# Kernel optimization log

Hardware: AMD Instinct MI355X
Metric: run time of the kernel (lower is better)

Reference implementation:

```python
import jax, jax.numpy as jnp
import numpy as np

NQ = 10          # num_qubits
NL = 4           # num_layers (StronglyEntanglingLayers)
DIM = 2 ** NQ    # state-vector dimension = input_linear out features
B = 4096
SEQ = 512
PRED = 96

# ---- static basis-state bookkeeping (wire 0 = most significant bit, as in PennyLane) ----

def _cnot_perm(control, target):
    s = np.arange(DIM)
    bit = (s >> (NQ - 1 - control)) & 1
    return s ^ (bit << (NQ - 1 - target))

def _layer_perms():
    # StronglyEntanglingLayers default ranges: r_l = (l % (n_wires - 1)) + 1,
    # then CNOT(i, (i+r) % n) for i = 0..n-1, applied sequentially.
    perms = []
    for l in range(NL):
        r = (l % (NQ - 1)) + 1
        comp = np.arange(DIM)
        for c in range(NQ):
            g = _cnot_perm(c, (c + r) % NQ)
            comp = comp[g]          # compose: state_new[t] = state_old[comp[t]]
        perms.append(jnp.asarray(comp))
    return perms

PERMS = _layer_perms()

_bits = (np.arange(DIM)[:, None] >> (NQ - 1 - np.arange(NQ))[None, :]) & 1
SIGNS = jnp.asarray(1.0 - 2.0 * _bits, dtype=np.float32)   # [DIM, NQ] PauliZ eigenvalues


def _rot_gates(w):
    # PennyLane Rot(phi, theta, omega) = RZ(omega) @ RY(theta) @ RZ(phi); w: [L, n, 3]
    phi, theta, omega = w[..., 0], w[..., 1], w[..., 2]
    c = jnp.cos(theta / 2)
    s = jnp.sin(theta / 2)
    ep = jnp.exp(0.5j * (phi + omega))   # e^{+i(phi+omega)/2}
    em = jnp.exp(0.5j * (phi - omega))   # e^{+i(phi-omega)/2}
    m00 = jnp.conj(ep) * c
    m01 = -em * s
    m10 = jnp.conj(em) * s
    m11 = ep * c
    return jnp.stack([jnp.stack([m00, m01], -1),
                      jnp.stack([m10, m11], -1)], -2)       # [L, n, 2, 2] complex64


def _apply_1q(psi, U, wire):
    # psi: [B, DIM] complex; apply 2x2 U on `wire`
    b = psi.shape[0]
    left = 2 ** wire
    right = 2 ** (NQ - 1 - wire)
    psi = psi.reshape(b, left, 2, right)
    psi = jnp.einsum('ba,kpaq->kpbq', U, psi)
    return psi.reshape(b, DIM)


def _circuit(psi, q_weights):
    mats = _rot_gates(q_weights)
    for l in range(NL):
        for w in range(NQ):
            psi = _apply_1q(psi, mats[l, w], w)
        psi = psi[:, PERMS[l]]          # composed CNOT ring of this layer
    return psi


def reference(x, W_in, b_in, q_weights, W_out, b_out):
    h = x @ W_in.T + b_in + 1e-6                          # input_linear, then +1e-6
    norm = jnp.linalg.norm(h, axis=-1, keepdims=True)
    psi = (h / norm).astype(jnp.complex64)                # AmplitudeEmbedding(normalize=True)
    psi = _circuit(psi, q_weights)                        # StronglyEntanglingLayers
    probs = psi.real ** 2 + psi.imag ** 2
    expvals = probs @ SIGNS                               # [B, NQ] PauliZ expvals
    return expvals @ W_out.T + b_out                      # output_linear


def setup_inputs() -> dict:
    key = jax.random.key(0)
    ks = jax.random.split(key, 6)
    x = jax.random.normal(ks[0], (B, SEQ), dtype=jnp.float32)
    W_in = jax.random.normal(ks[1], (DIM, SEQ), dtype=jnp.float32) / np.sqrt(SEQ)
    b_in = jax.random.normal(ks[2], (DIM,), dtype=jnp.float32) * 0.01
    q_weights = jax.random.uniform(ks[3], (NL, NQ, 3), dtype=jnp.float32,
                                   minval=0.0, maxval=2.0 * np.pi)
    W_out = jax.random.normal(ks[4], (PRED, NQ), dtype=jnp.float32) / np.sqrt(NQ)
    b_out = jax.random.normal(ks[5], (PRED,), dtype=jnp.float32) * 0.01
    return {"x": x, "W_in": W_in, "b_in": b_in, "q_weights": q_weights,
            "W_out": W_out, "b_out": b_out}
```

## Files before the change

kernel.cpp:

```cpp
#include <hip/hip_runtime.h>
#include <math.h>

#define DIM 1024
#define NQ 10
#define NL 4
#define SEQ 512
#define NROWS 4096
#define PRED 96

typedef unsigned short ushort_t;
typedef unsigned int uint_t;
using half8   = __attribute__((ext_vector_type(8))) _Float16;
using float4v = __attribute__((ext_vector_type(4))) float;

__device__ inline ushort_t f2h(float f) { _Float16 h = (_Float16)f; return *(ushort_t*)&h; }
__device__ inline uint_t pkh(float a, float b) {
    _Float16 ha = (_Float16)a, hb = (_Float16)b;
    return (uint_t)(*(ushort_t*)&ha) | ((uint_t)(*(ushort_t*)&hb) << 16);
}

__device__ inline int permf(int s, int r) {
#pragma unroll
    for (int c = 9; c >= 0; --c) {
        int t = (c + r) % 10;
        s ^= ((s >> (9 - c)) & 1) << (9 - t);
    }
    return s;
}

__global__ __launch_bounds__(64)
void circuit_wave64_kernel(const float* __restrict__ Wi, const float* __restrict__ b_in,
                           const float* __restrict__ qw,
                           ushort_t* __restrict__ Csm_r, ushort_t* __restrict__ Csm_i,
                           float* __restrict__ dr, float* __restrict__ di)
{
    __shared__ float gm[NL * NQ][8];
    __shared__ float2 wscr[1024];

    const int lane = threadIdx.x;
    const int jcol = blockIdx.x;

    if (lane < NL * NQ) {
        float phi = qw[lane * 3 + 0], theta = qw[lane * 3 + 1], omega = qw[lane * 3 + 2];
        float ch = cosf(theta * 0.5f), sh = sinf(theta * 0.5f);
        float a = 0.5f * (phi + omega), b = 0.5f * (phi - omega);
        float ca = cosf(a), sa = sinf(a);
        float cb = cosf(b), sb = sinf(b);
        gm[lane][0] =  ch * ca;  gm[lane][1] = -ch * sa;
        gm[lane][2] = -sh * cb;  gm[lane][3] = -sh * sb;
        gm[lane][4] =  sh * cb;  gm[lane][5] = -sh * sb;
        gm[lane][6] =  ch * ca;  gm[lane][7] =  ch * sa;
    }
    __syncthreads();

    float2 P[16];
    if (jcol < SEQ) {
#pragma unroll
        for (int r = 0; r < 16; ++r)
            P[r] = make_float2(Wi[(size_t)(lane * 16 + r) * SEQ + jcol], 0.f);
    } else {
#pragma unroll
        for (int r = 0; r < 16; ++r)
            P[r] = make_float2(b_in[lane * 16 + r] + 1e-6f, 0.f);
    }

#pragma unroll
    for (int l = 0; l < NL; ++l) {
#pragma unroll
        for (int w = 0; w < NQ; ++w) {
            const float* m = gm[l * NQ + w];
            float m00r = m[0], m00i = m[1], m01r = m[2], m01i = m[3];
            float m10r = m[4], m10i = m[5], m11r = m[6], m11i = m[7];
            if (w <= 5) {
                const int lb = 5 - w;
                const int mask = 1 << lb;
                const int myb = (lane >> lb) & 1;
                float cAr = myb ? m11r : m00r, cAi = myb ? m11i : m00i;
                float cQr = myb ? m10r : m01r, cQi = myb ? m10i : m01i;
#pragma unroll
                for (int r = 0; r < 16; ++r) {
                    float ar = P[r].x, ai = P[r].y;
                    float qr_ = __shfl_xor(ar, mask, 64);
                    float qi_ = __shfl_xor(ai, mask, 64);
                    P[r].x = cAr * ar - cAi * ai + cQr * qr_ - cQi * qi_;
                    P[r].y = cAr * ai + cAi * ar + cQr * qi_ + cQi * qr_;
                }
            } else {
                const int mk = 1 << (9 - w);
#pragma unroll
                for (int r0 = 0; r0 < 16; ++r0) {
                    if (r0 & mk) continue;
                    float2 a0 = P[r0], a1 = P[r0 | mk];
                    float2 n0, n1;
                    n0.x = m00r * a0.x - m00i * a0.y + m01r * a1.x - m01i * a1.y;
                    n0.y = m00r * a0.y + m00i * a0.x + m01r * a1.y + m01i * a1.x;
                    n1.x = m10r * a0.x - m10i * a0.y + m11r * a1.x - m11i * a1.y;
                    n1.y = m10r * a0.y + m10i * a0.x + m11r * a1.y + m11i * a1.x;
                    P[r0] = n0; P[r0 | mk] = n1;
                }
            }
        }
        const int rr = l % (NQ - 1) + 1;
        __syncthreads();
#pragma unroll
        for (int r = 0; r < 16; ++r) wscr[lane * 16 + r] = P[r];
        __syncthreads();
        int pl = permf(lane << 4, rr);
#pragma unroll
        for (int r = 0; r < 16; ++r) {
            int src = pl ^ permf(r, rr);
            P[r] = wscr[src];
        }
    }

    if (jcol < SEQ) {
#pragma unroll
        for (int r = 0; r < 16; ++r) {
            int s = lane * 16 + r;
            Csm_r[(size_t)s * SEQ + jcol] = f2h(P[r].x);
            Csm_i[(size_t)s * SEQ + jcol] = f2h(P[r].y);
        }
    } else {
#pragma unroll
        for (int r = 0; r < 16; ++r) {
            dr[lane * 16 + r] = P[r].x;
            di[lane * 16 + r] = P[r].y;
        }
    }
}

#define GBM 128
#define GBNC 64
#define GBK 32
#define LDA 40
#define LDP 65

__global__ __launch_bounds__(256)
void gemm_fused_kernel(const float* __restrict__ x,
                       const ushort_t* __restrict__ Crt_r, const ushort_t* __restrict__ Crt_i,
                       const float* __restrict__ dr, const float* __restrict__ di,
                       float* __restrict__ part)
{
    __shared__ __align__(16) char lds[GBM * LDP * 4];
    ushort_t* Ash = (ushort_t*)lds;
    ushort_t* Bsr = Ash + GBM * LDA;
    ushort_t* Bsi = Bsr + GBNC * LDA;
    float*    Ps  = (float*)lds;
    __shared__ float drs[GBNC], dis[GBNC];

    const int tid = threadIdx.x;
    const int bm = blockIdx.x, bn = blockIdx.y;
    const int lane = tid & 63, wv = tid >> 6;
    const int n0 = bn * GBNC;

    if (tid < GBNC) { drs[tid] = dr[n0 + tid]; dis[tid] = di[n0 + tid]; }

    float4v accr[2][4], acci[2][4];
#pragma unroll
    for (int a = 0; a < 2; ++a)
#pragma unroll
        for (int b = 0; b < 4; ++b) { accr[a][b] = (float4v)0.f; acci[a][b] = (float4v)0.f; }

    const int sr = tid >> 1, ko = (tid & 1) * 16;
    const float* xa = x + (size_t)(bm * GBM + sr) * SEQ + ko;
    const int bsel = tid >> 7;
    const int nr = (tid & 127) >> 1;
    const int bko = (tid & 1) * 16;
    const ushort_t* bsrc = (bsel ? Crt_i : Crt_r) + (size_t)(n0 + nr) * SEQ + bko;
    ushort_t* bdst = (bsel ? Bsi : Bsr) + nr * LDA + bko;

    const int fm = lane & 15, kq = (lane >> 4) * 8;
    const int wrow = wv * 32;

    for (int k0 = 0; k0 < SEQ; k0 += GBK) {
        float fv[16];
        *(float4*)&fv[0]  = *(const float4*)(xa + k0);
        *(float4*)&fv[4]  = *(const float4*)(xa + k0 + 4);
        *(float4*)&fv[8]  = *(const float4*)(xa + k0 + 8);
        *(float4*)&fv[12] = *(const float4*)(xa + k0 + 12);
        uint_t pk[8];
#pragma unroll
        for (int i = 0; i < 8; ++i) pk[i] = pkh(fv[2 * i], fv[2 * i + 1]);
        *(uint4*)(Ash + sr * LDA + ko)     = make_uint4(pk[0], pk[1], pk[2], pk[3]);
        *(uint4*)(Ash + sr * LDA + ko + 8) = make_uint4(pk[4], pk[5], pk[6], pk[7]);
        uint4 b0 = *(const uint4*)(bsrc + k0);
        uint4 b1 = *(const uint4*)(bsrc + k0 + 8);
        *(uint4*)bdst       = b0;
        *(uint4*)(bdst + 8) = b1;
        __syncthreads();

        half8 ah0 = *(half8*)(Ash + (wrow + fm) * LDA + kq);
        half8 ah1 = *(half8*)(Ash + (wrow + 16 + fm) * LDA + kq);
#pragma unroll
        for (int nt = 0; nt < 4; ++nt) {
            half8 br = *(half8*)(Bsr + (nt * 16 + fm) * LDA + kq);
            half8 bi = *(half8*)(Bsi + (nt * 16 + fm) * LDA + kq);
            accr[0][nt] = __builtin_amdgcn_mfma_f32_16x16x32_f16(ah0, br, accr[0][nt], 0, 0, 0);
            accr[1][nt] = __builtin_amdgcn_mfma_f32_16x16x32_f16(ah1, br, accr[1][nt], 0, 0, 0);
            acci[0][nt] = __builtin_amdgcn_mfma_f32_16x16x32_f16(ah0, bi, acci[0][nt], 0, 0, 0);
            acci[1][nt] = __builtin_amdgcn_mfma_f32_16x16x32_f16(ah1, bi, acci[1][nt], 0, 0, 0);
        }
        __syncthreads();
    }

    const int rq = (lane >> 4) * 4;
#pragma unroll
    for (int mt = 0; mt < 2; ++mt)
#pragma unroll
        for (int nt = 0; nt < 4; ++nt) {
            float drv = drs[nt * 16 + fm], div = dis[nt * 16 + fm];
#pragma unroll
            for (int reg = 0; reg < 4; ++reg) {
                int lrow = wrow + mt * 16 + rq + reg;
                float zr = accr[mt][nt][reg] + drv;
                float zi = acci[mt][nt][reg] + div;
                Ps[lrow * LDP + nt * 16 + fm] = zr * zr + zi * zi;
            }
        }
    __syncthreads();

    {
        const int row = tid >> 1, hh = tid & 1;
        const float* pr = Ps + row * LDP + hh * 32;
        float nrm = 0.f, e0 = 0.f, e1 = 0.f, e2 = 0.f, e3 = 0.f, e4 = 0.f, e5 = 0.f;
#pragma unroll
        for (int i = 0; i < 32; ++i) {
            float p = pr[i];
            int c = hh * 32 + i;
            nrm += p;
            e0 += ((c >> 5) & 1) ? -p : p;
            e1 += ((c >> 4) & 1) ? -p : p;
            e2 += ((c >> 3) & 1) ? -p : p;
            e3 += ((c >> 2) & 1) ? -p : p;
            e4 += ((c >> 1) & 1) ? -p : p;
            e5 += (c & 1) ? -p : p;
        }
        size_t base = ((size_t)(bm * GBM + row) * 32 + (bn * 2 + hh)) * 8;
        part[base + 0] = nrm;
        part[base + 1] = e0; part[base + 2] = e1; part[base + 3] = e2;
        part[base + 4] = e3; part[base + 5] = e4; part[base + 6] = e5;
    }
}

__global__ __launch_bounds__(128)
void finalize_kernel(const float* __restrict__ part, const float* __restrict__ W_out,
                     const float* __restrict__ b_out, float* __restrict__ out)
{
    __shared__ float evf[16];
    const int row = blockIdx.x, tid = threadIdx.x;

    if (tid < 64) {
        float v[11];
        if (tid < 32) {
            const float* p = part + ((size_t)row * 32 + tid) * 8;
            float4 a = *(const float4*)p;
            float4 b = *(const float4*)(p + 4);
            float nrm = a.x;
            int bnn = tid >> 1;
            v[0] = nrm;
            v[1] = (bnn & 8) ? -nrm : nrm;
            v[2] = (bnn & 4) ? -nrm : nrm;
            v[3] = (bnn & 2) ? -nrm : nrm;
            v[4] = (bnn & 1) ? -nrm : nrm;
            v[5] = a.y; v[6] = a.z; v[7] = a.w;
            v[8] = b.x; v[9] = b.y; v[10] = b.z;
        } else {
#pragma unroll
            for (int k = 0; k < 11; ++k) v[k] = 0.f;
        }
#pragma unroll
        for (int m = 16; m; m >>= 1)
#pragma unroll
            for (int k = 0; k < 11; ++k) v[k] += __shfl_xor(v[k], m, 64);
        if (tid == 0) {
            float inv = 1.0f / v[0];
#pragma unroll
            for (int k = 0; k < 10; ++k) evf[k] = v[k + 1] * inv;
        }
    }
    __syncthreads();
    if (tid < PRED) {
        float o = b_out[tid];
#pragma unroll
        for (int k = 0; k < NQ; ++k) o = fmaf(W_out[tid * NQ + k], evf[k], o);
        out[(size_t)row * PRED + tid] = o;
    }
}

extern "C" void kernel_launch(void* const* d_in, const int* in_sizes, int n_in,
                              void* d_out, int out_size, void* d_ws, size_t ws_size,
                              hipStream_t stream) {
    const float* x     = (const float*)d_in[0];
    const float* W_in  = (const float*)d_in[1];
    const float* b_in  = (const float*)d_in[2];
    const float* qw    = (const float*)d_in[3];
    const float* W_out = (const float*)d_in[4];
    const float* b_out = (const float*)d_in[5];
    float* out = (float*)d_out;

    char* w = (char*)d_ws;
    const size_t MB = 1u << 20;
    ushort_t* Csm_r = (ushort_t*)w;
    ushort_t* Csm_i = (ushort_t*)(w + 1 * MB);
    float*    dr    = (float*)(w + 2 * MB);
    float*    di    = dr + DIM;
    float*    part  = (float*)(w + 3 * MB);

    circuit_wave64_kernel<<<SEQ + 1, 64, 0, stream>>>(W_in, b_in, qw, Csm_r, Csm_i, dr, di);
    dim3 g2(NROWS / GBM, DIM / GBNC);
    gemm_fused_kernel<<<g2, 256, 0, stream>>>(x, Csm_r, Csm_i, dr, di, part);
    finalize_kernel<<<NROWS, 128, 0, stream>>>(part, W_out, b_out, out);
}
```

Measured before the change: 126.7 us.

## Transpose W_in and circuit output so circuit kernel uses coalesced vector accesses

Adds a tiled transpose kernel for W_in so each circuit block reads its column as contiguous float4 loads instead of strided scalar loads. The circuit kernel now writes its fp16 output in column-major order with packed 128-bit stores, and a second LDS-tiled transpose kernel converts it back to the layout the GEMM expects. This removes uncoalesced global traffic in the circuit kernel at the cost of two extra launches and extra round trips through workspace memory.

```diff
diff --git a/kernel.cpp b/kernel.cpp
--- a/kernel.cpp
+++ b/kernel.cpp
@@ -28,10 +28,37 @@
     return s;
 }
 
+__global__ __launch_bounds__(256)
+void transpose_win_kernel(const float* __restrict__ Wi, float* __restrict__ WiT)
+{
+    __shared__ float Ts[64][68];
+    const int tid = threadIdx.x;
+    const int k0 = blockIdx.x * 64;
+    const int j0 = blockIdx.y * 64;
+
+    const int jj = (tid & 15) * 4;
+    const int kk = tid >> 4;
+#pragma unroll
+    for (int i = 0; i < 4; ++i) {
+        int k = kk + i * 16;
+        float4 v = *(const float4*)(Wi + (size_t)(k0 + k) * SEQ + j0 + jj);
+        Ts[k][jj] = v.x; Ts[k][jj + 1] = v.y; Ts[k][jj + 2] = v.z; Ts[k][jj + 3] = v.w;
+    }
+    __syncthreads();
+    const int kk2 = (tid & 15) * 4;
+    const int jj2 = tid >> 4;
+#pragma unroll
+    for (int i = 0; i < 4; ++i) {
+        int j = jj2 + i * 16;
+        float4 v = make_float4(Ts[kk2][j], Ts[kk2 + 1][j], Ts[kk2 + 2][j], Ts[kk2 + 3][j]);
+        *(float4*)(WiT + (size_t)(j0 + j) * DIM + k0 + kk2) = v;
+    }
+}
+
 __global__ __launch_bounds__(64)
-void circuit_wave64_kernel(const float* __restrict__ Wi, const float* __restrict__ b_in,
+void circuit_wave64_kernel(const float* __restrict__ WiT, const float* __restrict__ b_in,
                            const float* __restrict__ qw,
-                           ushort_t* __restrict__ Csm_r, ushort_t* __restrict__ Csm_i,
+                           ushort_t* __restrict__ Cjm_r, ushort_t* __restrict__ Cjm_i,
                            float* __restrict__ dr, float* __restrict__ di)
 {
     __shared__ float gm[NL * NQ][8];
@@ -55,9 +82,19 @@
 
     float2 P[16];
     if (jcol < SEQ) {
-#pragma unroll
-        for (int r = 0; r < 16; ++r)
-            P[r] = make_float2(Wi[(size_t)(lane * 16 + r) * SEQ + jcol], 0.f);
+        const float* src = WiT + (size_t)jcol * DIM + lane * 16;
+        float4 v0 = *(const float4*)(src);
+        float4 v1 = *(const float4*)(src + 4);
+        float4 v2 = *(const float4*)(src + 8);
+        float4 v3 = *(const float4*)(src + 12);
+        P[0]  = make_float2(v0.x, 0.f); P[1]  = make_float2(v0.y, 0.f);
+        P[2]  = make_float2(v0.z, 0.f); P[3]  = make_float2(v0.w, 0.f);
+        P[4]  = make_float2(v1.x, 0.f); P[5]  = make_float2(v1.y, 0.f);
+        P[6]  = make_float2(v1.z, 0.f); P[7]  = make_float2(v1.w, 0.f);
+        P[8]  = make_float2(v2.x, 0.f); P[9]  = make_float2(v2.y, 0.f);
+        P[10] = make_float2(v2.z, 0.f); P[11] = make_float2(v2.w, 0.f);
+        P[12] = make_float2(v3.x, 0.f); P[13] = make_float2(v3.y, 0.f);
+        P[14] = make_float2(v3.z, 0.f); P[15] = make_float2(v3.w, 0.f);
     } else {
 #pragma unroll
         for (int r = 0; r < 16; ++r)
@@ -114,18 +151,59 @@
     }
 
     if (jcol < SEQ) {
-#pragma unroll
-        for (int r = 0; r < 16; ++r) {
-            int s = lane * 16 + r;
-            Csm_r[(size_t)s * SEQ + jcol] = f2h(P[r].x);
-            Csm_i[(size_t)s * SEQ + jcol] = f2h(P[r].y);
-        }
+        uint4 o0, o1, p0, p1;
+        o0.x = pkh(P[0].x,  P[1].x);  o0.y = pkh(P[2].x,  P[3].x);
+        o0.z = pkh(P[4].x,  P[5].x);  o0.w = pkh(P[6].x,  P[7].x);
+        o1.x = pkh(P[8].x,  P[9].x);  o1.y = pkh(P[10].x, P[11].x);
+        o1.z = pkh(P[12].x, P[13].x); o1.w = pkh(P[14].x, P[15].x);
+        p0.x = pkh(P[0].y,  P[1].y);  p0.y = pkh(P[2].y,  P[3].y);
+        p0.z = pkh(P[4].y,  P[5].y);  p0.w = pkh(P[6].y,  P[7].y);
+        p1.x = pkh(P[8].y,  P[9].y);  p1.y = pkh(P[10].y, P[11].y);
+        p1.z = pkh(P[12].y, P[13].y); p1.w = pkh(P[14].y, P[15].y);
+        size_t base = (size_t)jcol * DIM + lane * 16;
+        *(uint4*)(Cjm_r + base)     = o0;
+        *(uint4*)(Cjm_r + base + 8) = o1;
+        *(uint4*)(Cjm_i + base)     = p0;
+        *(uint4*)(Cjm_i + base + 8) = p1;
     } else {
 #pragma unroll
         for (int r = 0; r < 16; ++r) {
             dr[lane * 16 + r] = P[r].x;
             di[lane * 16 + r] = P[r].y;
         }
+    }
+}
+
+__global__ __launch_bounds__(256)
+void transpose_c_kernel(const ushort_t* __restrict__ in_r, const ushort_t* __restrict__ in_i,
+                        ushort_t* __restrict__ out_r, ushort_t* __restrict__ out_i)
+{
+    __shared__ ushort_t Ts[64][80];
+    const int tid = threadIdx.x;
+    const int j0 = blockIdx.x * 64;
+    const int s0 = blockIdx.y * 64;
+
+    for (int a = 0; a < 2; ++a) {
+        const ushort_t* in = a ? in_i : in_r;
+        ushort_t* out = a ? out_i : out_r;
+#pragma unroll
+        for (int g = 0; g < 2; ++g) {
+            int G = tid + g * 256;
+            int jj = G >> 3, ch = G & 7;
+            uint4 v = *(const uint4*)(in + (size_t)(j0 + jj) * DIM + s0 + ch * 8);
+            const ushort_t* hv = (const ushort_t*)&v;
+#pragma unroll
+            for (int q = 0; q < 8; ++q) Ts[ch * 8 + q][jj] = hv[q];
+        }
+        __syncthreads();
+#pragma unroll
+        for (int g = 0; g < 2; ++g) {
+            int G = tid + g * 256;
+            int ss = G >> 3, jc = G & 7;
+            uint4 v = *(const uint4*)(&Ts[ss][jc * 8]);
+            *(uint4*)(out + (size_t)(s0 + ss) * SEQ + j0 + jc * 8) = v;
+        }
+        __syncthreads();
     }
 }
 
@@ -300,13 +378,18 @@
 
     char* w = (char*)d_ws;
     const size_t MB = 1u << 20;
-    ushort_t* Csm_r = (ushort_t*)w;
-    ushort_t* Csm_i = (ushort_t*)(w + 1 * MB);
-    float*    dr    = (float*)(w + 2 * MB);
+    float*    WiT   = (float*)w;
+    ushort_t* Cjm_r = (ushort_t*)(w + 2 * MB);
+    ushort_t* Cjm_i = (ushort_t*)(w + 3 * MB);
+    ushort_t* Csm_r = (ushort_t*)(w + 4 * MB);
+    ushort_t* Csm_i = (ushort_t*)(w + 5 * MB);
+    float*    dr    = (float*)(w + 6 * MB);
     float*    di    = dr + DIM;
-    float*    part  = (float*)(w + 3 * MB);
-
-    circuit_wave64_kernel<<<SEQ + 1, 64, 0, stream>>>(W_in, b_in, qw, Csm_r, Csm_i, dr, di);
+    float*    part  = (float*)(w + 7 * MB);
+
+    transpose_win_kernel<<<dim3(DIM / 64, SEQ / 64), 256, 0, stream>>>(W_in, WiT);
+    circuit_wave64_kernel<<<SEQ + 1, 64, 0, stream>>>(WiT, b_in, qw, Cjm_r, Cjm_i, dr, di);
+    transpose_c_kernel<<<dim3(SEQ / 64, DIM / 64), 256, 0, stream>>>(Cjm_r, Cjm_i, Csm_r, Csm_i);
     dim3 g2(NROWS / GBM, DIM / GBNC);
     gemm_fused_kernel<<<g2, 256, 0, stream>>>(x, Csm_r, Csm_i, dr, di, part);
     finalize_kernel<<<NROWS, 128, 0, stream>>>(part, W_out, b_out, out);
```

Result: no change. 124.6 us (-1.7%).
